# Performance work log

Hardware: AMD Instinct MI355X
Metric: run time of the kernel (lower is better)

Reference implementation:

```python
import jax, jax.numpy as jnp
import numpy as np

D = 512  # c_size == q_size


def setup_inputs() -> dict:
    key = jax.random.key(0)
    ks = jax.random.split(key, 8)
    c = jax.random.normal(ks[0], (8, 2048, D), dtype=jnp.float32)
    q = jax.random.normal(ks[1], (8, 512, D), dtype=jnp.float32)
    sc = 1.0 / np.sqrt(D)
    w_c = jax.random.uniform(ks[2], (D,), jnp.float32, -sc, sc)
    b_c = jax.random.uniform(ks[3], (), jnp.float32, -sc, sc)
    w_q = jax.random.uniform(ks[4], (D,), jnp.float32, -sc, sc)
    b_q = jax.random.uniform(ks[5], (), jnp.float32, -sc, sc)
    w_cq = jax.random.uniform(ks[6], (D,), jnp.float32, -sc, sc)
    b_cq = jax.random.uniform(ks[7], (), jnp.float32, -sc, sc)
    return {"c": c, "q": q, "w_c": w_c, "b_c": b_c, "w_q": w_q, "b_q": b_q,
            "w_cq": w_cq, "b_cq": b_cq}


def reference(c, q, w_c, b_c, w_q, b_q, w_cq, b_cq):
    # s[b,t,i] = <c[b,t],w_c>+b_c + <q[b,i],w_q>+b_q + <c[b,t]*q[b,i], w_cq>+b_cq
    # The original per-query-token loop for att_weight_cq(c*qi) collapses to
    # a single batched contraction since the Linear is linear in c*qi.
    sc = jnp.einsum('btd,d->bt', c, w_c) + b_c          # (B, c_len)
    sq = jnp.einsum('bid,d->bi', q, w_q) + b_q          # (B, q_len)
    scq = jnp.einsum('btd,bid->bti', c * w_cq, q) + b_cq  # (B, c_len, q_len)
    s = sc[:, :, None] + sq[:, None, :] + scq

    a = jax.nn.softmax(s, axis=2)                       # attend over q
    c2q = jnp.einsum('bti,bid->btd', a, q)              # (B, c_len, D)

    b = jax.nn.softmax(jnp.max(s, axis=2), axis=1)      # (B, c_len)
    q2c = jnp.einsum('bt,btd->bd', b, c)                # (B, D)
    q2c = jnp.broadcast_to(q2c[:, None, :], c.shape)    # (B, c_len, D)

    x = jnp.concatenate([c, c2q, c * c2q, c * q2c], axis=-1)
    return x
```

## Files before the change

kernel.cpp:

```cpp
#include <hip/hip_runtime.h>
#include <cstdint>


constexpr int kB = 8;
constexpr int kT = 2048;
constexpr int kI = 512;
constexpr int kD = 512;
constexpr int kW = 4 * kD;
constexpr int kRows = 64;
constexpr int kTiles = kT / kRows;
constexpr int kChunk = kRows * 72;

using f32x4  = __attribute__((ext_vector_type(4))) float;
using bf16x4 = __attribute__((ext_vector_type(4))) __bf16;
using bf16x8 = __attribute__((ext_vector_type(8))) __bf16;

__device__ __forceinline__ float dot8(const f32x4& a0, const f32x4& a1,
                                      const f32x4& b0, const f32x4& b1) {
  return a0.x * b0.x + a0.y * b0.y + a0.z * b0.z + a0.w * b0.w +
         a1.x * b1.x + a1.y * b1.y + a1.z * b1.z + a1.w * b1.w;
}

__global__ __launch_bounds__(256) void prep_qf_kernel(
    const float* __restrict__ q, const float* __restrict__ w_q,
    const float* __restrict__ b_q, float* __restrict__ sq,
    __bf16* __restrict__ qf) {
  __shared__ float sacc[16][17];
  const int b = blockIdx.y;
  const int g = blockIdx.x;
  const int tid = threadIdx.x;
  const int kk0 = tid >> 6;
  const int lane = tid & 63;
  const int lr = lane & 15, lg = lane >> 4;
  const float* row = q + ((size_t)(b * kI + g * 16 + lr)) * kD;
  float sp = 0.f;
#pragma unroll
  for (int kk = kk0; kk < 16; kk += 4) {
    const int ka = kk * 32 + lg * 8;
    f32x4 v0 = *(const f32x4*)(row + ka);
    f32x4 v1 = *(const f32x4*)(row + ka + 4);
    f32x4 u0 = *(const f32x4*)(w_q + ka);
    f32x4 u1 = *(const f32x4*)(w_q + ka + 4);
    sp += dot8(v0, v1, u0, u1);
    bf16x8 o = {(__bf16)v0.x, (__bf16)v0.y, (__bf16)v0.z, (__bf16)v0.w,
                (__bf16)v1.x, (__bf16)v1.y, (__bf16)v1.z, (__bf16)v1.w};
    *(bf16x8*)(qf + ((((size_t)(b * 32 + g)) * 16 + kk) << 9) + lane * 8) = o;
  }
  sacc[lr][kk0 * 4 + lg] = sp;
  __syncthreads();
  if (tid < 16) {
    float s = 0.f;
#pragma unroll
    for (int j = 0; j < 16; ++j) s += sacc[tid][j];
    sq[b * kI + g * 16 + tid] = s + b_q[0];
  }
}

__global__ __launch_bounds__(256) void prep_vf_kernel(
    const float* __restrict__ q, __bf16* __restrict__ vf) {
  __shared__ float ts[64][68];
  const int b = blockIdx.z;
  const int i0 = blockIdx.x * 64;
  const int d0 = blockIdx.y * 64;
  const int tid = threadIdx.x;
  const int r = tid >> 2;
  const int cg = (tid & 3) * 16;
#pragma unroll
  for (int j = 0; j < 4; ++j) {
    f32x4 v = *(const f32x4*)(q + ((size_t)(b * kI + i0 + r)) * kD + d0 + cg + 4 * j);
    ts[r][cg + 4 * j + 0] = v.x;
    ts[r][cg + 4 * j + 1] = v.y;
    ts[r][cg + 4 * j + 2] = v.z;
    ts[r][cg + 4 * j + 3] = v.w;
  }
  __syncthreads();
  const int dl = tid >> 2;
  const int ig = (tid & 3) * 16;
  bf16x8 o0, o1;
#pragma unroll
  for (int j = 0; j < 8; ++j) o0[j] = (__bf16)ts[ig + j][dl];
#pragma unroll
  for (int j = 0; j < 8; ++j) o1[j] = (__bf16)ts[ig + 8 + j][dl];
  const int gd = (d0 >> 4) + (dl >> 4);
  const int lr = dl & 15;
  const int kki0 = (i0 >> 5) + (ig >> 5);
  const int lg0 = (ig & 31) >> 3;
  const int i1 = ig + 8;
  const int kki1 = (i0 >> 5) + (i1 >> 5);
  const int lg1 = (i1 & 31) >> 3;
  *(bf16x8*)(vf + ((((size_t)(b * 32 + gd)) * 16 + kki0) << 9) +
             (lg0 * 16 + lr) * 8) = o0;
  *(bf16x8*)(vf + ((((size_t)(b * 32 + gd)) * 16 + kki1) << 9) +
             (lg1 * 16 + lr) * 8) = o1;
}

__global__ __launch_bounds__(512, 2) void fused_attn(
    const float* __restrict__ c, const __bf16* __restrict__ qf,
    const __bf16* __restrict__ vf, const float* __restrict__ w_cq,
    const float* __restrict__ w_c, const float* __restrict__ b_c,
    const float* __restrict__ b_cq, const float* __restrict__ sq,
    float* __restrict__ out, float* __restrict__ mz,
    float* __restrict__ u_tile) {
  __shared__ __align__(16) char lAP[16 * kChunk];
  __shared__ float scrow[kRows];
  __shared__ float redm[8 * kRows];
  __shared__ float reds[8 * kRows];

  const int b = blockIdx.y;
  const int tile = blockIdx.x;
  const int t0 = tile * kRows;
  const int tid = threadIdx.x;
  const int w = tid >> 6;
  const int lane = tid & 63;
  const int lr = lane & 15, lg = lane >> 4;

  const int srow = tid >> 3;
  const int col4 = (tid & 7) * 4;
  const float* crow = c + ((size_t)(b * kT + t0 + srow)) * kD;
  float* orow0 = out + ((size_t)(b * kT + t0 + srow)) * kW;
  float scp = 0.f;

  f32x4 c1, c2;
  {
    f32x4 c0 = *(const f32x4*)(crow + col4);
    c1 = *(const f32x4*)(crow + 32 + col4);
    const f32x4 wq = *(const f32x4*)(w_cq + col4);
    const f32x4 wc = *(const f32x4*)(w_c + col4);
    *(f32x4*)(orow0 + col4) = c0;
    scp += c0.x * wc.x + c0.y * wc.y + c0.z * wc.z + c0.w * wc.w;
    c0 *= wq;
    bf16x4 bv = {(__bf16)c0.x, (__bf16)c0.y, (__bf16)c0.z, (__bf16)c0.w};
    *(bf16x4*)(lAP + 0 * kChunk + srow * 72 + col4 * 2) = bv;
  }

  const __bf16* qfb = qf + (((size_t)(b * 32 + w * 4)) * 16 << 9) + lane * 8;
  f32x4 acc[4][4] = {};
  bf16x8 b0[4], b1[4], b2[4];
#pragma unroll
  for (int n4 = 0; n4 < 4; ++n4)
    b0[n4] = *(const bf16x8*)(qfb + (((size_t)(n4 * 16 + 0)) << 9));
#pragma unroll
  for (int n4 = 0; n4 < 4; ++n4)
    b1[n4] = *(const bf16x8*)(qfb + (((size_t)(n4 * 16 + 1)) << 9));
  __syncthreads();

#pragma unroll
  for (int kk = 0; kk < 16; ++kk) {
    if (kk < 14) c2 = *(const f32x4*)(crow + (kk + 2) * 32 + col4);
    if (kk < 14) {
#pragma unroll
      for (int n4 = 0; n4 < 4; ++n4)
        b2[n4] = *(const bf16x8*)(qfb + (((size_t)(n4 * 16 + kk + 2)) << 9));
    }
    bf16x8 af[4];
#pragma unroll
    for (int m = 0; m < 4; ++m)
      af[m] = *(const bf16x8*)(lAP + kk * kChunk + (m * 16 + lr) * 72 + lg * 16);
#pragma unroll
    for (int m = 0; m < 4; ++m)
#pragma unroll
      for (int n4 = 0; n4 < 4; ++n4)
        acc[m][n4] = __builtin_amdgcn_mfma_f32_16x16x32_bf16(af[m], b0[n4],
                                                             acc[m][n4], 0, 0, 0);
    if (kk < 15) {
      const int col = (kk + 1) * 32 + col4;
      const f32x4 wq = *(const f32x4*)(w_cq + col);
      const f32x4 wc = *(const f32x4*)(w_c + col);
      *(f32x4*)(orow0 + col) = c1;
      scp += c1.x * wc.x + c1.y * wc.y + c1.z * wc.z + c1.w * wc.w;
      f32x4 vv = c1 * wq;
      bf16x4 bv = {(__bf16)vv.x, (__bf16)vv.y, (__bf16)vv.z, (__bf16)vv.w};
      *(bf16x4*)(lAP + (kk + 1) * kChunk + srow * 72 + col4 * 2) = bv;
      c1 = c2;
    }
#pragma unroll
    for (int n4 = 0; n4 < 4; ++n4) {
      b0[n4] = b1[n4];
      b1[n4] = b2[n4];
    }
    __syncthreads();
  }

  scp += __shfl_xor(scp, 1, 64);
  scp += __shfl_xor(scp, 2, 64);
  scp += __shfl_xor(scp, 4, 64);
  if ((tid & 7) == 0) scrow[srow] = scp + b_c[0];
  __syncthreads();

  const float bq = b_cq[0];
  float sqv[4];
#pragma unroll
  for (int n4 = 0; n4 < 4; ++n4) sqv[n4] = sq[b * kI + w * 64 + n4 * 16 + lr];
  float scr[4][4];
#pragma unroll
  for (int m = 0; m < 4; ++m)
#pragma unroll
    for (int r = 0; r < 4; ++r) scr[m][r] = scrow[m * 16 + lg * 4 + r] + bq;
#pragma unroll
  for (int m = 0; m < 4; ++m)
#pragma unroll
    for (int n4 = 0; n4 < 4; ++n4)
#pragma unroll
      for (int r = 0; r < 4; ++r) acc[m][n4][r] += scr[m][r] + sqv[n4];

  float mx[4][4];
#pragma unroll
  for (int m = 0; m < 4; ++m)
#pragma unroll
    for (int r = 0; r < 4; ++r) {
      float v = acc[m][0][r];
#pragma unroll
      for (int n4 = 1; n4 < 4; ++n4) v = fmaxf(v, acc[m][n4][r]);
#pragma unroll
      for (int off = 1; off <= 8; off <<= 1) v = fmaxf(v, __shfl_xor(v, off, 64));
      mx[m][r] = v;
    }
  if (lr == 0) {
#pragma unroll
    for (int m = 0; m < 4; ++m)
#pragma unroll
      for (int r = 0; r < 4; ++r)
        redm[w * kRows + m * 16 + lg * 4 + r] = mx[m][r];
  }
  __syncthreads();
#pragma unroll
  for (int m = 0; m < 4; ++m)
#pragma unroll
    for (int r = 0; r < 4; ++r) {
      const int rw = m * 16 + lg * 4 + r;
      float v = redm[rw];
#pragma unroll
      for (int w2 = 1; w2 < 8; ++w2) v = fmaxf(v, redm[w2 * kRows + rw]);
      mx[m][r] = v;
    }

  float sm[4][4] = {};
#pragma unroll
  for (int m = 0; m < 4; ++m)
#pragma unroll
    for (int n4 = 0; n4 < 4; ++n4)
#pragma unroll
      for (int r = 0; r < 4; ++r) {
        const float p = __expf(acc[m][n4][r] - mx[m][r]);
        acc[m][n4][r] = p;
        sm[m][r] += p;
      }
#pragma unroll
  for (int m = 0; m < 4; ++m)
#pragma unroll
    for (int r = 0; r < 4; ++r)
#pragma unroll
      for (int off = 1; off <= 8; off <<= 1)
        sm[m][r] += __shfl_xor(sm[m][r], off, 64);
  if (lr == 0) {
#pragma unroll
    for (int m = 0; m < 4; ++m)
#pragma unroll
      for (int r = 0; r < 4; ++r)
        reds[w * kRows + m * 16 + lg * 4 + r] = sm[m][r];
  }
  __syncthreads();
  float inv[4][4];
#pragma unroll
  for (int m = 0; m < 4; ++m)
#pragma unroll
    for (int r = 0; r < 4; ++r) {
      const int rw = m * 16 + lg * 4 + r;
      float v = reds[rw];
#pragma unroll
      for (int w2 = 1; w2 < 8; ++w2) v += reds[w2 * kRows + rw];
      inv[m][r] = 1.f / v;
    }

  const __bf16* vfb = vf + (((size_t)(b * 32 + w * 4)) * 16 << 9) + lane * 8;
  bf16x8 v0_[4], v1_[4], v2_[4];
#pragma unroll
  for (int n4 = 0; n4 < 4; ++n4)
    v0_[n4] = *(const bf16x8*)(vfb + (((size_t)(n4 * 16 + 0)) << 9));
#pragma unroll
  for (int n4 = 0; n4 < 4; ++n4)
    v1_[n4] = *(const bf16x8*)(vfb + (((size_t)(n4 * 16 + 1)) << 9));

#pragma unroll
  for (int m = 0; m < 4; ++m)
#pragma unroll
    for (int r = 0; r < 4; ++r) {
      const int trow = m * 16 + lg * 4 + r;
#pragma unroll
      for (int n4 = 0; n4 < 4; ++n4) {
        const int icol = w * 64 + n4 * 16 + lr;
        const int kkc = icol >> 5, kc = icol & 31;
        *(__bf16*)(lAP + kkc * kChunk + trow * 72 + kc * 2) =
            (__bf16)(acc[m][n4][r] * inv[m][r]);
      }
    }
  __syncthreads();

  f32x4 o[4][4] = {};
#pragma unroll
  for (int kki = 0; kki < 16; ++kki) {
    if (kki < 14) {
#pragma unroll
      for (int n4 = 0; n4 < 4; ++n4)
        v2_[n4] = *(const bf16x8*)(vfb + (((size_t)(n4 * 16 + kki + 2)) << 9));
    }
    bf16x8 af[4];
#pragma unroll
    for (int m = 0; m < 4; ++m)
      af[m] = *(const bf16x8*)(lAP + kki * kChunk + (m * 16 + lr) * 72 + lg * 16);
#pragma unroll
    for (int m = 0; m < 4; ++m)
#pragma unroll
      for (int n4 = 0; n4 < 4; ++n4)
        o[m][n4] = __builtin_amdgcn_mfma_f32_16x16x32_bf16(af[m], v0_[n4],
                                                           o[m][n4], 0, 0, 0);
#pragma unroll
    for (int n4 = 0; n4 < 4; ++n4) {
      v0_[n4] = v1_[n4];
      v1_[n4] = v2_[n4];
    }
  }

  float m_tile;
  {
    float v = mx[0][0];
#pragma unroll
    for (int m = 0; m < 4; ++m)
#pragma unroll
      for (int r = 0; r < 4; ++r) v = fmaxf(v, mx[m][r]);
    v = fmaxf(v, __shfl_xor(v, 16, 64));
    v = fmaxf(v, __shfl_xor(v, 32, 64));
    m_tile = v;
  }
  float u[4] = {};
  float zz = 0.f;
#pragma unroll
  for (int m = 0; m < 4; ++m)
#pragma unroll
    for (int r = 0; r < 4; ++r) {
      const int t = t0 + m * 16 + lg * 4 + r;
      const size_t rb = (size_t)(b * kT + t);
      float* orow = out + rb * kW;
      const float ev = __expf(mx[m][r] - m_tile);
      zz += ev;
#pragma unroll
      for (int n4 = 0; n4 < 4; ++n4) {
        const int d = w * 64 + n4 * 16 + lr;
        const float cvv = orow[d];
        const float pv = o[m][n4][r];
        orow[kD + d] = pv;
        orow[2 * kD + d] = cvv * pv;
        u[n4] += ev * cvv;
      }
    }
#pragma unroll
  for (int n4 = 0; n4 < 4; ++n4) {
    u[n4] += __shfl_xor(u[n4], 16, 64);
    u[n4] += __shfl_xor(u[n4], 32, 64);
  }
  if (lg == 0) {
    float* ub = u_tile + ((size_t)(b * kTiles + tile)) * kD;
#pragma unroll
    for (int n4 = 0; n4 < 4; ++n4) ub[w * 64 + n4 * 16 + lr] = u[n4];
  }
  if (w == 0) {
    zz += __shfl_xor(zz, 16, 64);
    zz += __shfl_xor(zz, 32, 64);
    if (lane == 0) {
      mz[b * 64 + tile] = m_tile;
      mz[b * 64 + 32 + tile] = zz;
    }
  }
}

__global__ __launch_bounds__(512) void slot3_merge_kernel(
    const float* __restrict__ c, const float* __restrict__ mz,
    const float* __restrict__ u_tile, float* __restrict__ out) {
  const int b = blockIdx.y;
  const int tile = blockIdx.x;
  const int t0 = tile * kRows;
  const int tid = threadIdx.x;
  __shared__ float sM[32], sZ[32];
  __shared__ float sq2c[kD];
  if (tid < 32) {
    sM[tid] = mz[b * 64 + tid];
    sZ[tid] = mz[b * 64 + 32 + tid];
  }
  __syncthreads();
  {
    float M = sM[0];
#pragma unroll
    for (int k = 1; k < 32; ++k) M = fmaxf(M, sM[k]);
    float Z = 0.f;
    float s = 0.f;
#pragma unroll
    for (int k = 0; k < 32; ++k) {
      const float wk = __expf(sM[k] - M);
      Z += wk * sZ[k];
      s += wk * u_tile[((size_t)(b * kTiles + k)) * kD + tid];
    }
    sq2c[tid] = s / Z;
  }
  __syncthreads();
  const int srow = tid >> 3;
  const int col4 = (tid & 7) * 4;
  const size_t rb = (size_t)(b * kT + t0 + srow);
  const float* crow = c + rb * kD;
  float* orow3 = out + rb * kW + 3 * kD;
#pragma unroll
  for (int j = 0; j < 16; ++j) {
    const int col = col4 + j * 32;
    const f32x4 cv = *(const f32x4*)(crow + col);
    const f32x4 qc = *(const f32x4*)(sq2c + col);
    *(f32x4*)(orow3 + col) = cv * qc;
  }
}

extern "C" void kernel_launch(void* const* d_in, const int* in_sizes, int n_in,
                              void* d_out, int out_size, void* d_ws, size_t ws_size,
                              hipStream_t stream) {
  const float* c    = (const float*)d_in[0];
  const float* q    = (const float*)d_in[1];
  const float* w_c  = (const float*)d_in[2];
  const float* b_c  = (const float*)d_in[3];
  const float* w_q  = (const float*)d_in[4];
  const float* b_q  = (const float*)d_in[5];
  const float* w_cq = (const float*)d_in[6];
  const float* b_cq = (const float*)d_in[7];
  float* out = (float*)d_out;
  float* ws = (float*)d_ws;

  float* sq     = ws;
  float* mz     = sq + kB * kI;
  float* u_tile = mz + kB * 64;
  __bf16* qf = (__bf16*)(u_tile + (size_t)kB * kTiles * kD);
  __bf16* vf = qf + (size_t)kB * kI * kD;

  dim3 gpq(kI / 16, kB);
  prep_qf_kernel<<<gpq, 256, 0, stream>>>(q, w_q, b_q, sq, qf);
  dim3 gpv(kI / 64, kD / 64, kB);
  prep_vf_kernel<<<gpv, 256, 0, stream>>>(q, vf);

  dim3 gf(kTiles, kB);
  fused_attn<<<gf, 512, 0, stream>>>(c, qf, vf, w_cq, w_c, b_c, b_cq, sq, out,
                                     mz, u_tile);

  slot3_merge_kernel<<<gf, 512, 0, stream>>>(c, mz, u_tile, out);
}
```

Baseline: 72.92 us.

## Merge prep kernels, stage whole C tile upfront, deepen B prefetch

```diff
diff --git a/kernel.cpp b/kernel.cpp
--- a/kernel.cpp
+++ b/kernel.cpp
@@ -21,77 +21,75 @@
          a1.x * b1.x + a1.y * b1.y + a1.z * b1.z + a1.w * b1.w;
 }
 
-__global__ __launch_bounds__(256) void prep_qf_kernel(
+__global__ __launch_bounds__(256) void prep_kernel(
     const float* __restrict__ q, const float* __restrict__ w_q,
     const float* __restrict__ b_q, float* __restrict__ sq,
-    __bf16* __restrict__ qf) {
-  __shared__ float sacc[16][17];
+    __bf16* __restrict__ qf, __bf16* __restrict__ vf) {
   const int b = blockIdx.y;
-  const int g = blockIdx.x;
   const int tid = threadIdx.x;
-  const int kk0 = tid >> 6;
-  const int lane = tid & 63;
-  const int lr = lane & 15, lg = lane >> 4;
-  const float* row = q + ((size_t)(b * kI + g * 16 + lr)) * kD;
-  float sp = 0.f;
-#pragma unroll
-  for (int kk = kk0; kk < 16; kk += 4) {
-    const int ka = kk * 32 + lg * 8;
-    f32x4 v0 = *(const f32x4*)(row + ka);
-    f32x4 v1 = *(const f32x4*)(row + ka + 4);
-    f32x4 u0 = *(const f32x4*)(w_q + ka);
-    f32x4 u1 = *(const f32x4*)(w_q + ka + 4);
-    sp += dot8(v0, v1, u0, u1);
-    bf16x8 o = {(__bf16)v0.x, (__bf16)v0.y, (__bf16)v0.z, (__bf16)v0.w,
-                (__bf16)v1.x, (__bf16)v1.y, (__bf16)v1.z, (__bf16)v1.w};
-    *(bf16x8*)(qf + ((((size_t)(b * 32 + g)) * 16 + kk) << 9) + lane * 8) = o;
-  }
-  sacc[lr][kk0 * 4 + lg] = sp;
-  __syncthreads();
-  if (tid < 16) {
-    float s = 0.f;
-#pragma unroll
-    for (int j = 0; j < 16; ++j) s += sacc[tid][j];
-    sq[b * kI + g * 16 + tid] = s + b_q[0];
-  }
-}
-
-__global__ __launch_bounds__(256) void prep_vf_kernel(
-    const float* __restrict__ q, __bf16* __restrict__ vf) {
-  __shared__ float ts[64][68];
-  const int b = blockIdx.z;
-  const int i0 = blockIdx.x * 64;
-  const int d0 = blockIdx.y * 64;
-  const int tid = threadIdx.x;
-  const int r = tid >> 2;
-  const int cg = (tid & 3) * 16;
-#pragma unroll
-  for (int j = 0; j < 4; ++j) {
-    f32x4 v = *(const f32x4*)(q + ((size_t)(b * kI + i0 + r)) * kD + d0 + cg + 4 * j);
-    ts[r][cg + 4 * j + 0] = v.x;
-    ts[r][cg + 4 * j + 1] = v.y;
-    ts[r][cg + 4 * j + 2] = v.z;
-    ts[r][cg + 4 * j + 3] = v.w;
-  }
-  __syncthreads();
-  const int dl = tid >> 2;
-  const int ig = (tid & 3) * 16;
-  bf16x8 o0, o1;
-#pragma unroll
-  for (int j = 0; j < 8; ++j) o0[j] = (__bf16)ts[ig + j][dl];
-#pragma unroll
-  for (int j = 0; j < 8; ++j) o1[j] = (__bf16)ts[ig + 8 + j][dl];
-  const int gd = (d0 >> 4) + (dl >> 4);
-  const int lr = dl & 15;
-  const int kki0 = (i0 >> 5) + (ig >> 5);
-  const int lg0 = (ig & 31) >> 3;
-  const int i1 = ig + 8;
-  const int kki1 = (i0 >> 5) + (i1 >> 5);
-  const int lg1 = (i1 & 31) >> 3;
-  *(bf16x8*)(vf + ((((size_t)(b * 32 + gd)) * 16 + kki0) << 9) +
-             (lg0 * 16 + lr) * 8) = o0;
-  *(bf16x8*)(vf + ((((size_t)(b * 32 + gd)) * 16 + kki1) << 9) +
-             (lg1 * 16 + lr) * 8) = o1;
+  if (blockIdx.x < 32) {
+    __shared__ float sacc[16][17];
+    const int g = blockIdx.x;
+    const int kk0 = tid >> 6;
+    const int lane = tid & 63;
+    const int lr = lane & 15, lg = lane >> 4;
+    const float* row = q + ((size_t)(b * kI + g * 16 + lr)) * kD;
+    float sp = 0.f;
+#pragma unroll
+    for (int kk = kk0; kk < 16; kk += 4) {
+      const int ka = kk * 32 + lg * 8;
+      f32x4 v0 = *(const f32x4*)(row + ka);
+      f32x4 v1 = *(const f32x4*)(row + ka + 4);
+      f32x4 u0 = *(const f32x4*)(w_q + ka);
+      f32x4 u1 = *(const f32x4*)(w_q + ka + 4);
+      sp += dot8(v0, v1, u0, u1);
+      bf16x8 o = {(__bf16)v0.x, (__bf16)v0.y, (__bf16)v0.z, (__bf16)v0.w,
+                  (__bf16)v1.x, (__bf16)v1.y, (__bf16)v1.z, (__bf16)v1.w};
+      *(bf16x8*)(qf + ((((size_t)(b * 32 + g)) * 16 + kk) << 9) + lane * 8) = o;
+    }
+    sacc[lr][kk0 * 4 + lg] = sp;
+    __syncthreads();
+    if (tid < 16) {
+      float s = 0.f;
+#pragma unroll
+      for (int j = 0; j < 16; ++j) s += sacc[tid][j];
+      sq[b * kI + g * 16 + tid] = s + b_q[0];
+    }
+  } else {
+    __shared__ float ts[64][68];
+    const int blk = blockIdx.x - 32;
+    const int i0 = (blk & 7) * 64;
+    const int d0 = (blk >> 3) * 64;
+    const int r = tid >> 2;
+    const int cg = (tid & 3) * 16;
+#pragma unroll
+    for (int j = 0; j < 4; ++j) {
+      f32x4 v = *(const f32x4*)(q + ((size_t)(b * kI + i0 + r)) * kD + d0 + cg + 4 * j);
+      ts[r][cg + 4 * j + 0] = v.x;
+      ts[r][cg + 4 * j + 1] = v.y;
+      ts[r][cg + 4 * j + 2] = v.z;
+      ts[r][cg + 4 * j + 3] = v.w;
+    }
+    __syncthreads();
+    const int dl = tid >> 2;
+    const int ig = (tid & 3) * 16;
+    bf16x8 o0, o1;
+#pragma unroll
+    for (int j = 0; j < 8; ++j) o0[j] = (__bf16)ts[ig + j][dl];
+#pragma unroll
+    for (int j = 0; j < 8; ++j) o1[j] = (__bf16)ts[ig + 8 + j][dl];
+    const int gd = (d0 >> 4) + (dl >> 4);
+    const int lr = dl & 15;
+    const int kki0 = (i0 >> 5) + (ig >> 5);
+    const int lg0 = (ig & 31) >> 3;
+    const int i1 = ig + 8;
+    const int kki1 = (i0 >> 5) + (i1 >> 5);
+    const int lg1 = (i1 & 31) >> 3;
+    *(bf16x8*)(vf + ((((size_t)(b * 32 + gd)) * 16 + kki0) << 9) +
+               (lg0 * 16 + lr) * 8) = o0;
+    *(bf16x8*)(vf + ((((size_t)(b * 32 + gd)) * 16 + kki1) << 9) +
+               (lg1 * 16 + lr) * 8) = o1;
+  }
 }
 
 __global__ __launch_bounds__(512, 2) void fused_attn(
@@ -114,43 +112,50 @@
   const int lane = tid & 63;
   const int lr = lane & 15, lg = lane >> 4;
 
-  const int srow = tid >> 3;
-  const int col4 = (tid & 7) * 4;
-  const float* crow = c + ((size_t)(b * kT + t0 + srow)) * kD;
-  float* orow0 = out + ((size_t)(b * kT + t0 + srow)) * kW;
-  float scp = 0.f;
-
-  f32x4 c1, c2;
+  const __bf16* qfb = qf + (((size_t)(b * 32 + w * 4)) * 16 << 9) + lane * 8;
+  bf16x8 b0[4], b1[4], b2[4], b3[4];
+#pragma unroll
+  for (int n4 = 0; n4 < 4; ++n4)
+    b0[n4] = *(const bf16x8*)(qfb + (((size_t)(n4 * 16 + 0)) << 9));
+#pragma unroll
+  for (int n4 = 0; n4 < 4; ++n4)
+    b1[n4] = *(const bf16x8*)(qfb + (((size_t)(n4 * 16 + 1)) << 9));
+#pragma unroll
+  for (int n4 = 0; n4 < 4; ++n4)
+    b2[n4] = *(const bf16x8*)(qfb + (((size_t)(n4 * 16 + 2)) << 9));
+
   {
-    f32x4 c0 = *(const f32x4*)(crow + col4);
-    c1 = *(const f32x4*)(crow + 32 + col4);
-    const f32x4 wq = *(const f32x4*)(w_cq + col4);
-    const f32x4 wc = *(const f32x4*)(w_c + col4);
-    *(f32x4*)(orow0 + col4) = c0;
-    scp += c0.x * wc.x + c0.y * wc.y + c0.z * wc.z + c0.w * wc.w;
-    c0 *= wq;
-    bf16x4 bv = {(__bf16)c0.x, (__bf16)c0.y, (__bf16)c0.z, (__bf16)c0.w};
-    *(bf16x4*)(lAP + 0 * kChunk + srow * 72 + col4 * 2) = bv;
-  }
-
-  const __bf16* qfb = qf + (((size_t)(b * 32 + w * 4)) * 16 << 9) + lane * 8;
+    const int srow = tid >> 3;
+    const int col4 = (tid & 7) * 4;
+    const float* crow = c + ((size_t)(b * kT + t0 + srow)) * kD;
+    float* orow0 = out + ((size_t)(b * kT + t0 + srow)) * kW;
+    float scp = 0.f;
+#pragma unroll
+    for (int j = 0; j < 16; ++j) {
+      const int col = col4 + j * 32;
+      f32x4 v = *(const f32x4*)(crow + col);
+      *(f32x4*)(orow0 + col) = v;
+      const f32x4 wq = *(const f32x4*)(w_cq + col);
+      const f32x4 wc = *(const f32x4*)(w_c + col);
+      scp += v.x * wc.x + v.y * wc.y + v.z * wc.z + v.w * wc.w;
+      v *= wq;
+      bf16x4 bv = {(__bf16)v.x, (__bf16)v.y, (__bf16)v.z, (__bf16)v.w};
+      *(bf16x4*)(lAP + j * kChunk + srow * 72 + col4 * 2) = bv;
+    }
+    scp += __shfl_xor(scp, 1, 64);
+    scp += __shfl_xor(scp, 2, 64);
+    scp += __shfl_xor(scp, 4, 64);
+    if ((tid & 7) == 0) scrow[srow] = scp + b_c[0];
+  }
+  __syncthreads();
+
   f32x4 acc[4][4] = {};
-  bf16x8 b0[4], b1[4], b2[4];
-#pragma unroll
-  for (int n4 = 0; n4 < 4; ++n4)
-    b0[n4] = *(const bf16x8*)(qfb + (((size_t)(n4 * 16 + 0)) << 9));
-#pragma unroll
-  for (int n4 = 0; n4 < 4; ++n4)
-    b1[n4] = *(const bf16x8*)(qfb + (((size_t)(n4 * 16 + 1)) << 9));
-  __syncthreads();
-
 #pragma unroll
   for (int kk = 0; kk < 16; ++kk) {
-    if (kk < 14) c2 = *(const f32x4*)(crow + (kk + 2) * 32 + col4);
-    if (kk < 14) {
+    if (kk < 13) {
 #pragma unroll
       for (int n4 = 0; n4 < 4; ++n4)
-        b2[n4] = *(const bf16x8*)(qfb + (((size_t)(n4 * 16 + kk + 2)) << 9));
+        b3[n4] = *(const bf16x8*)(qfb + (((size_t)(n4 * 16 + kk + 3)) << 9));
     }
     bf16x8 af[4];
 #pragma unroll
@@ -162,30 +167,13 @@
       for (int n4 = 0; n4 < 4; ++n4)
         acc[m][n4] = __builtin_amdgcn_mfma_f32_16x16x32_bf16(af[m], b0[n4],
                                                              acc[m][n4], 0, 0, 0);
-    if (kk < 15) {
-      const int col = (kk + 1) * 32 + col4;
-      const f32x4 wq = *(const f32x4*)(w_cq + col);
-      const f32x4 wc = *(const f32x4*)(w_c + col);
-      *(f32x4*)(orow0 + col) = c1;
-      scp += c1.x * wc.x + c1.y * wc.y + c1.z * wc.z + c1.w * wc.w;
-      f32x4 vv = c1 * wq;
-      bf16x4 bv = {(__bf16)vv.x, (__bf16)vv.y, (__bf16)vv.z, (__bf16)vv.w};
-      *(bf16x4*)(lAP + (kk + 1) * kChunk + srow * 72 + col4 * 2) = bv;
-      c1 = c2;
-    }
 #pragma unroll
     for (int n4 = 0; n4 < 4; ++n4) {
       b0[n4] = b1[n4];
       b1[n4] = b2[n4];
-    }
-    __syncthreads();
-  }
-
-  scp += __shfl_xor(scp, 1, 64);
-  scp += __shfl_xor(scp, 2, 64);
-  scp += __shfl_xor(scp, 4, 64);
-  if ((tid & 7) == 0) scrow[srow] = scp + b_c[0];
-  __syncthreads();
+      b2[n4] = b3[n4];
+    }
+  }
 
   const float bq = b_cq[0];
   float sqv[4];
@@ -273,13 +261,16 @@
     }
 
   const __bf16* vfb = vf + (((size_t)(b * 32 + w * 4)) * 16 << 9) + lane * 8;
-  bf16x8 v0_[4], v1_[4], v2_[4];
+  bf16x8 v0_[4], v1_[4], v2_[4], v3_[4];
 #pragma unroll
   for (int n4 = 0; n4 < 4; ++n4)
     v0_[n4] = *(const bf16x8*)(vfb + (((size_t)(n4 * 16 + 0)) << 9));
 #pragma unroll
   for (int n4 = 0; n4 < 4; ++n4)
     v1_[n4] = *(const bf16x8*)(vfb + (((size_t)(n4 * 16 + 1)) << 9));
+#pragma unroll
+  for (int n4 = 0; n4 < 4; ++n4)
+    v2_[n4] = *(const bf16x8*)(vfb + (((size_t)(n4 * 16 + 2)) << 9));
 
 #pragma unroll
   for (int m = 0; m < 4; ++m)
@@ -299,10 +290,10 @@
   f32x4 o[4][4] = {};
 #pragma unroll
   for (int kki = 0; kki < 16; ++kki) {
-    if (kki < 14) {
+    if (kki < 13) {
 #pragma unroll
       for (int n4 = 0; n4 < 4; ++n4)
-        v2_[n4] = *(const bf16x8*)(vfb + (((size_t)(n4 * 16 + kki + 2)) << 9));
+        v3_[n4] = *(const bf16x8*)(vfb + (((size_t)(n4 * 16 + kki + 3)) << 9));
     }
     bf16x8 af[4];
 #pragma unroll
@@ -318,6 +309,7 @@
     for (int n4 = 0; n4 < 4; ++n4) {
       v0_[n4] = v1_[n4];
       v1_[n4] = v2_[n4];
+      v2_[n4] = v3_[n4];
     }
   }
 
@@ -374,8 +366,8 @@
 }
 
 __global__ __launch_bounds__(512) void slot3_merge_kernel(
-    const float* __restrict__ c, const float* __restrict__ mz,
-    const float* __restrict__ u_tile, float* __restrict__ out) {
+    const float* __restrict__ mz, const float* __restrict__ u_tile,
+    float* __restrict__ out) {
   const int b = blockIdx.y;
   const int tile = blockIdx.x;
   const int t0 = tile * kRows;
@@ -405,14 +397,13 @@
   const int srow = tid >> 3;
   const int col4 = (tid & 7) * 4;
   const size_t rb = (size_t)(b * kT + t0 + srow);
-  const float* crow = c + rb * kD;
-  float* orow3 = out + rb * kW + 3 * kD;
+  float* orow = out + rb * kW;
 #pragma unroll
   for (int j = 0; j < 16; ++j) {
     const int col = col4 + j * 32;
-    const f32x4 cv = *(const f32x4*)(crow + col);
+    const f32x4 cv = *(const f32x4*)(orow + col);
     const f32x4 qc = *(const f32x4*)(sq2c + col);
-    *(f32x4*)(orow3 + col) = cv * qc;
+    *(f32x4*)(orow + 3 * kD + col) = cv * qc;
   }
 }
 
@@ -436,14 +427,12 @@
   __bf16* qf = (__bf16*)(u_tile + (size_t)kB * kTiles * kD);
   __bf16* vf = qf + (size_t)kB * kI * kD;
 
-  dim3 gpq(kI / 16, kB);
-  prep_qf_kernel<<<gpq, 256, 0, stream>>>(q, w_q, b_q, sq, qf);
-  dim3 gpv(kI / 64, kD / 64, kB);
-  prep_vf_kernel<<<gpv, 256, 0, stream>>>(q, vf);
+  dim3 gp(96, kB);
+  prep_kernel<<<gp, 256, 0, stream>>>(q, w_q, b_q, sq, qf, vf);
 
   dim3 gf(kTiles, kB);
   fused_attn<<<gf, 512, 0, stream>>>(c, qf, vf, w_cq, w_c, b_c, b_cq, sq, out,
                                      mz, u_tile);
 
-  slot3_merge_kernel<<<gf, 512, 0, stream>>>(c, mz, u_tile, out);
+  slot3_merge_kernel<<<gf, 512, 0, stream>>>(mz, u_tile, out);
 }
```

Result: faster. 71.21 us (-2.4%).
